# Kernel tuning notes

Hardware: AMD Instinct MI355X
Metric: run time of the kernel (lower is better)

Reference implementation:

```python
import jax, jax.numpy as jnp
import numpy as np


def _pairwise_sq_dists(x, y):
    # x: (B, N, 3), y: (B, M, 3) -> (B, N, M) squared L2 distances
    xx = jnp.sum(x * x, axis=2)                      # (B, N)
    yy = jnp.sum(y * y, axis=2)                      # (B, M)
    xy = jnp.einsum('bnd,bmd->bnm', x, y)            # (B, N, M)
    d = xx[:, :, None] + yy[:, None, :] - 2.0 * xy
    return jnp.maximum(d, 0.0)


def setup_inputs() -> dict:
    key = jax.random.key(0)
    k1, k2 = jax.random.split(key)
    B, N, M = 16, 4096, 4096
    pred = jax.random.normal(k1, (B, N, 3), dtype=jnp.float32)
    target = jax.random.normal(k2, (B, M, 3), dtype=jnp.float32)
    return {"pred": pred, "target": target}


def reference(pred, target):
    # ChamferLoss(use_l1=False, symmetry_weight=0.0), reduce='mean'
    d = _pairwise_sq_dists(pred, target)             # (B, N, M)
    min_p2t = jnp.min(d, axis=2)                     # (B, N)
    min_t2p = jnp.min(d, axis=1)                     # (B, M)
    per_sample = jnp.mean(min_p2t, axis=1) + jnp.mean(min_t2p, axis=1)  # (B,)
    return jnp.mean(per_sample)
```

## Files before the change

kernel.cpp:

```cpp
#include <hip/hip_runtime.h>
#include <math.h>

#define NPTS   4096
#define BATCH  16
#define BLK    512
#define CS     4
#define COLS_PER_BLK (NPTS / CS)
#define TPB    (COLS_PER_BLK / 32)
#define PANELS 16

typedef __attribute__((ext_vector_type(8)))  short bf16x8;
typedef __attribute__((ext_vector_type(16))) float f32x16;

static __device__ __forceinline__ unsigned short f2bf(float x) {
    unsigned u = __float_as_uint(x);
    unsigned r = 0x7FFFu + ((u >> 16) & 1u);
    return (unsigned short)((u + r) >> 16);
}
static __device__ __forceinline__ float bf2f(unsigned short h) {
    return __uint_as_float(((unsigned)h) << 16);
}
static __device__ __forceinline__ float min3f(float a, float b, float c) {
    return fminf(fminf(a, b), c);
}


__global__ __launch_bounds__(BLK) void chamfer_mfma(
    const float* __restrict__ pred, const float* __restrict__ target,
    unsigned* __restrict__ gcolmin, unsigned* __restrict__ growmin)
{
    __shared__ __align__(16) bf16x8 sB[TPB * 64];
    __shared__ unsigned colmin[COLS_PER_BLK];

    const int bx    = blockIdx.x;
    const int cs    = bx & (CS - 1);
    const int panel = bx >> 2;
    const int b     = blockIdx.y;
    const int t     = threadIdx.x;
    const int w     = t >> 6;
    const int l     = t & 63;
    const short one = (short)0x3F80;

    for (int i = t; i < COLS_PER_BLK; i += BLK) colmin[i] = 0x7F800000u;

    const int colbase = cs * COLS_PER_BLK;
    for (int e = t; e < TPB * 64; e += BLK) {
        const int el   = e & 63;
        const int tile = e >> 6;
        const int col  = colbase + tile * 32 + (el & 31);
        const float* tp = target + ((size_t)b * NPTS + col) * 3;
        float x = tp[0], y = tp[1], z = tp[2];
        unsigned short hx = f2bf(x), hy = f2bf(y), hz = f2bf(z);
        unsigned short lx = f2bf(x - bf2f(hx));
        unsigned short ly = f2bf(y - bf2f(hy));
        unsigned short lz = f2bf(z - bf2f(hz));
        float tt = fmaf(z, z, fmaf(y, y, x * x));
        unsigned short th = f2bf(tt);
        unsigned short tl = f2bf(tt - bf2f(th));
        bf16x8 v;
        if (el < 32)
            v = (bf16x8){(short)hx, (short)hy, (short)hz,
                         (short)hx, (short)hy, (short)hz,
                         (short)lx, (short)ly};
        else
            v = (bf16x8){(short)lz, one, one, (short)th, (short)tl, 0, 0, 0};
        sB[e] = v;
    }

    const int r   = l & 31;
    const int row = panel * 256 + w * 32 + r;
    const float* pp_ = pred + ((size_t)b * NPTS + row) * 3;
    float x = pp_[0], y = pp_[1], z = pp_[2];
    unsigned short hx = f2bf(x), hy = f2bf(y), hz = f2bf(z);
    unsigned short lx = f2bf(x - bf2f(hx));
    unsigned short ly = f2bf(y - bf2f(hy));
    unsigned short lz = f2bf(z - bf2f(hz));
    unsigned short n2hx = f2bf(-2.0f * bf2f(hx));
    unsigned short n2hy = f2bf(-2.0f * bf2f(hy));
    unsigned short n2hz = f2bf(-2.0f * bf2f(hz));
    unsigned short n2lx = f2bf(-2.0f * bf2f(lx));
    unsigned short n2ly = f2bf(-2.0f * bf2f(ly));
    unsigned short n2lz = f2bf(-2.0f * bf2f(lz));
    float pp = fmaf(z, z, fmaf(y, y, x * x));
    unsigned short pph = f2bf(pp);
    unsigned short ppl = f2bf(pp - bf2f(pph));
    bf16x8 afrag;
    if (l < 32)
        afrag = (bf16x8){(short)n2hx, (short)n2hy, (short)n2hz,
                         (short)n2lx, (short)n2ly, (short)n2lz,
                         (short)n2hx, (short)n2hy};
    else
        afrag = (bf16x8){(short)n2hz, (short)pph, (short)ppl, one, one, 0, 0, 0};

    __syncthreads();

    f32x16 rmin;
    #pragma unroll
    for (int i = 0; i < 16; ++i) rmin[i] = INFINITY;
    f32x16 zacc;
    #pragma unroll
    for (int i = 0; i < 16; ++i) zacc[i] = 0.0f;

    #pragma unroll 2
    for (int tile = 0; tile < TPB; ++tile) {
        bf16x8 bft = sB[tile * 64 + l];
        f32x16 acc = __builtin_amdgcn_mfma_f32_32x32x16_bf16(afrag, bft, zacc, 0, 0, 0);

        #pragma unroll
        for (int i = 0; i < 16; ++i) rmin[i] = fminf(rmin[i], acc[i]);

        float t0 = min3f(acc[0],  acc[1],  acc[2]);
        float t1 = min3f(acc[3],  acc[4],  acc[5]);
        float t2 = min3f(acc[6],  acc[7],  acc[8]);
        float t3 = min3f(acc[9],  acc[10], acc[11]);
        float t4 = min3f(acc[12], acc[13], acc[14]);
        float m  = fminf(min3f(t0, t1, t2), min3f(t3, t4, acc[15]));
        atomicMin(&colmin[tile * 32 + r], __float_as_uint(fmaxf(m, 0.0f)));
    }

    #pragma unroll
    for (int i = 0; i < 16; ++i) {
        float v = rmin[i];
        v = fminf(v, __shfl_xor(v, 1, 64));
        v = fminf(v, __shfl_xor(v, 2, 64));
        v = fminf(v, __shfl_xor(v, 4, 64));
        v = fminf(v, __shfl_xor(v, 8, 64));
        v = fminf(v, __shfl_xor(v, 16, 64));
        rmin[i] = v;
    }
    if ((l & 31) == 0) {
        const int h = l >> 5;
        unsigned* rb = growmin + (size_t)b * NPTS + panel * 256 + w * 32;
        #pragma unroll
        for (int i = 0; i < 16; ++i) {
            const int rloc = (i & 3) + 8 * (i >> 2) + 4 * h;
            atomicMin(&rb[rloc], __float_as_uint(fmaxf(rmin[i], 0.0f)));
        }
    }

    __syncthreads();
    unsigned* cb = gcolmin + (size_t)b * NPTS + colbase;
    for (int i = t; i < COLS_PER_BLK; i += BLK)
        atomicMin(&cb[i], colmin[i]);
}

__global__ __launch_bounds__(256) void chamfer_sum(
    const uint4* __restrict__ mins, float* __restrict__ out)
{
    __shared__ float wsum[4];
    const int gid = blockIdx.x * 256 + threadIdx.x;

    float s = 0.0f;
    for (int i = gid; i < (2 * BATCH * NPTS) / 4; i += 8192) {
        uint4 v = mins[i];
        s += __uint_as_float(v.x) + __uint_as_float(v.y)
           + __uint_as_float(v.z) + __uint_as_float(v.w);
    }

    #pragma unroll
    for (int off = 32; off > 0; off >>= 1)
        s += __shfl_down(s, off, 64);

    if ((threadIdx.x & 63) == 0) wsum[threadIdx.x >> 6] = s;
    __syncthreads();

    if (threadIdx.x == 0) {
        float acc = wsum[0] + wsum[1] + wsum[2] + wsum[3];
        atomicAdd(out, acc * (1.0f / ((float)BATCH * (float)NPTS)));
    }
}

extern "C" void kernel_launch(void* const* d_in, const int* in_sizes, int n_in,
                              void* d_out, int out_size, void* d_ws, size_t ws_size,
                              hipStream_t stream) {
    const float* pred   = (const float*)d_in[0];
    const float* target = (const float*)d_in[1];
    float* out = (float*)d_out;

    unsigned* gcolmin = (unsigned*)d_ws;
    unsigned* growmin = gcolmin + (size_t)BATCH * NPTS;

    hipMemsetAsync(d_ws, 0x7F, (size_t)2 * BATCH * NPTS * 4, stream);
    hipMemsetAsync(out, 0, sizeof(float), stream);

    chamfer_mfma<<<dim3(CS * PANELS, BATCH), BLK, 0, stream>>>(
        pred, target, gcolmin, growmin);
    chamfer_sum<<<dim3(32), 256, 0, stream>>>((const uint4*)d_ws, out);
}
```

Baseline: 82.71 us.

## Compute both Chamfer directions as row-min passes, drop atomics and memset

Instead of getting column minima through per-tile shared atomics, the kernel now adds a grid z dimension so each direction (pred→target and target→pred) runs as a pure row-min pass. Each wave holds two A fragments covering 64 rows, so every shared B tile load feeds two MFMAs. Per-column-split partial minima are written plainly, and the sum kernel folds the four splits, which removes the global atomicMin traffic and the workspace memset. The price is that the MFMA work doubles, since each pairwise distance is now computed once per direction.

```diff
diff --git a/kernel.cpp b/kernel.cpp
--- a/kernel.cpp
+++ b/kernel.cpp
@@ -7,7 +7,8 @@
 #define CS     4
 #define COLS_PER_BLK (NPTS / CS)
 #define TPB    (COLS_PER_BLK / 32)
-#define PANELS 16
+#define ROWS_PER_BLK 512
+#define PANELS (NPTS / ROWS_PER_BLK)
 
 typedef __attribute__((ext_vector_type(8)))  short bf16x8;
 typedef __attribute__((ext_vector_type(16))) float f32x16;
@@ -20,35 +21,57 @@
 static __device__ __forceinline__ float bf2f(unsigned short h) {
     return __uint_as_float(((unsigned)h) << 16);
 }
-static __device__ __forceinline__ float min3f(float a, float b, float c) {
-    return fminf(fminf(a, b), c);
+
+
+static __device__ __forceinline__ bf16x8 make_afrag(const float* mp, int l) {
+    const short one = (short)0x3F80;
+    float x = mp[0], y = mp[1], z = mp[2];
+    unsigned short hx = f2bf(x), hy = f2bf(y), hz = f2bf(z);
+    unsigned short lx = f2bf(x - bf2f(hx));
+    unsigned short ly = f2bf(y - bf2f(hy));
+    unsigned short lz = f2bf(z - bf2f(hz));
+    unsigned short n2hx = f2bf(-2.0f * bf2f(hx));
+    unsigned short n2hy = f2bf(-2.0f * bf2f(hy));
+    unsigned short n2hz = f2bf(-2.0f * bf2f(hz));
+    unsigned short n2lx = f2bf(-2.0f * bf2f(lx));
+    unsigned short n2ly = f2bf(-2.0f * bf2f(ly));
+    unsigned short n2lz = f2bf(-2.0f * bf2f(lz));
+    float pp = fmaf(z, z, fmaf(y, y, x * x));
+    unsigned short pph = f2bf(pp);
+    unsigned short ppl = f2bf(pp - bf2f(pph));
+    if (l < 32)
+        return (bf16x8){(short)n2hx, (short)n2hy, (short)n2hz,
+                        (short)n2lx, (short)n2ly, (short)n2lz,
+                        (short)n2hx, (short)n2hy};
+    else
+        return (bf16x8){(short)n2hz, (short)pph, (short)ppl, one, one, 0, 0, 0};
 }
-
 
 __global__ __launch_bounds__(BLK) void chamfer_mfma(
     const float* __restrict__ pred, const float* __restrict__ target,
-    unsigned* __restrict__ gcolmin, unsigned* __restrict__ growmin)
+    float* __restrict__ partial)
 {
     __shared__ __align__(16) bf16x8 sB[TPB * 64];
-    __shared__ unsigned colmin[COLS_PER_BLK];
 
     const int bx    = blockIdx.x;
     const int cs    = bx & (CS - 1);
     const int panel = bx >> 2;
     const int b     = blockIdx.y;
+    const int dir   = blockIdx.z;
     const int t     = threadIdx.x;
     const int w     = t >> 6;
     const int l     = t & 63;
     const short one = (short)0x3F80;
 
-    for (int i = t; i < COLS_PER_BLK; i += BLK) colmin[i] = 0x7F800000u;
+    const float* mine  = dir ? target : pred;
+    const float* other = dir ? pred : target;
 
     const int colbase = cs * COLS_PER_BLK;
     for (int e = t; e < TPB * 64; e += BLK) {
         const int el   = e & 63;
         const int tile = e >> 6;
         const int col  = colbase + tile * 32 + (el & 31);
-        const float* tp = target + ((size_t)b * NPTS + col) * 3;
+        const float* tp = other + ((size_t)b * NPTS + col) * 3;
         float x = tp[0], y = tp[1], z = tp[2];
         unsigned short hx = f2bf(x), hy = f2bf(y), hz = f2bf(z);
         unsigned short lx = f2bf(x - bf2f(hx));
@@ -67,94 +90,72 @@
         sB[e] = v;
     }
 
-    const int r   = l & 31;
-    const int row = panel * 256 + w * 32 + r;
-    const float* pp_ = pred + ((size_t)b * NPTS + row) * 3;
-    float x = pp_[0], y = pp_[1], z = pp_[2];
-    unsigned short hx = f2bf(x), hy = f2bf(y), hz = f2bf(z);
-    unsigned short lx = f2bf(x - bf2f(hx));
-    unsigned short ly = f2bf(y - bf2f(hy));
-    unsigned short lz = f2bf(z - bf2f(hz));
-    unsigned short n2hx = f2bf(-2.0f * bf2f(hx));
-    unsigned short n2hy = f2bf(-2.0f * bf2f(hy));
-    unsigned short n2hz = f2bf(-2.0f * bf2f(hz));
-    unsigned short n2lx = f2bf(-2.0f * bf2f(lx));
-    unsigned short n2ly = f2bf(-2.0f * bf2f(ly));
-    unsigned short n2lz = f2bf(-2.0f * bf2f(lz));
-    float pp = fmaf(z, z, fmaf(y, y, x * x));
-    unsigned short pph = f2bf(pp);
-    unsigned short ppl = f2bf(pp - bf2f(pph));
-    bf16x8 afrag;
-    if (l < 32)
-        afrag = (bf16x8){(short)n2hx, (short)n2hy, (short)n2hz,
-                         (short)n2lx, (short)n2ly, (short)n2lz,
-                         (short)n2hx, (short)n2hy};
-    else
-        afrag = (bf16x8){(short)n2hz, (short)pph, (short)ppl, one, one, 0, 0, 0};
+    const int rowbase = panel * ROWS_PER_BLK + w * 64;
+    const size_t mb = (size_t)b * NPTS;
+    bf16x8 af[2];
+    #pragma unroll
+    for (int j = 0; j < 2; ++j)
+        af[j] = make_afrag(mine + (mb + rowbase + j * 32 + (l & 31)) * 3, l);
 
     __syncthreads();
 
-    f32x16 rmin;
+    f32x16 rm[2];
     #pragma unroll
-    for (int i = 0; i < 16; ++i) rmin[i] = INFINITY;
+    for (int j = 0; j < 2; ++j)
+        #pragma unroll
+        for (int i = 0; i < 16; ++i) rm[j][i] = INFINITY;
+
     f32x16 zacc;
     #pragma unroll
     for (int i = 0; i < 16; ++i) zacc[i] = 0.0f;
 
-    #pragma unroll 2
     for (int tile = 0; tile < TPB; ++tile) {
         bf16x8 bft = sB[tile * 64 + l];
-        f32x16 acc = __builtin_amdgcn_mfma_f32_32x32x16_bf16(afrag, bft, zacc, 0, 0, 0);
-
+        f32x16 a0 = __builtin_amdgcn_mfma_f32_32x32x16_bf16(af[0], bft, zacc, 0, 0, 0);
+        f32x16 a1 = __builtin_amdgcn_mfma_f32_32x32x16_bf16(af[1], bft, zacc, 0, 0, 0);
         #pragma unroll
-        for (int i = 0; i < 16; ++i) rmin[i] = fminf(rmin[i], acc[i]);
-
-        float t0 = min3f(acc[0],  acc[1],  acc[2]);
-        float t1 = min3f(acc[3],  acc[4],  acc[5]);
-        float t2 = min3f(acc[6],  acc[7],  acc[8]);
-        float t3 = min3f(acc[9],  acc[10], acc[11]);
-        float t4 = min3f(acc[12], acc[13], acc[14]);
-        float m  = fminf(min3f(t0, t1, t2), min3f(t3, t4, acc[15]));
-        atomicMin(&colmin[tile * 32 + r], __float_as_uint(fmaxf(m, 0.0f)));
+        for (int i = 0; i < 16; ++i) rm[0][i] = fminf(rm[0][i], a0[i]);
+        #pragma unroll
+        for (int i = 0; i < 16; ++i) rm[1][i] = fminf(rm[1][i], a1[i]);
     }
 
+    const int h = l >> 5;
+    float* pb = partial + (((size_t)dir * BATCH + b) * CS + cs) * NPTS;
     #pragma unroll
-    for (int i = 0; i < 16; ++i) {
-        float v = rmin[i];
-        v = fminf(v, __shfl_xor(v, 1, 64));
-        v = fminf(v, __shfl_xor(v, 2, 64));
-        v = fminf(v, __shfl_xor(v, 4, 64));
-        v = fminf(v, __shfl_xor(v, 8, 64));
-        v = fminf(v, __shfl_xor(v, 16, 64));
-        rmin[i] = v;
-    }
-    if ((l & 31) == 0) {
-        const int h = l >> 5;
-        unsigned* rb = growmin + (size_t)b * NPTS + panel * 256 + w * 32;
+    for (int j = 0; j < 2; ++j) {
         #pragma unroll
         for (int i = 0; i < 16; ++i) {
-            const int rloc = (i & 3) + 8 * (i >> 2) + 4 * h;
-            atomicMin(&rb[rloc], __float_as_uint(fmaxf(rmin[i], 0.0f)));
+            float v = rm[j][i];
+            v = fminf(v, __shfl_xor(v, 1, 64));
+            v = fminf(v, __shfl_xor(v, 2, 64));
+            v = fminf(v, __shfl_xor(v, 4, 64));
+            v = fminf(v, __shfl_xor(v, 8, 64));
+            v = fminf(v, __shfl_xor(v, 16, 64));
+            rm[j][i] = v;
+        }
+        if ((l & 31) == 0) {
+            #pragma unroll
+            for (int i = 0; i < 16; ++i) {
+                const int row = rowbase + j * 32 + (i & 3) + 8 * (i >> 2) + 4 * h;
+                pb[row] = rm[j][i];
+            }
         }
     }
-
-    __syncthreads();
-    unsigned* cb = gcolmin + (size_t)b * NPTS + colbase;
-    for (int i = t; i < COLS_PER_BLK; i += BLK)
-        atomicMin(&cb[i], colmin[i]);
 }
 
 __global__ __launch_bounds__(256) void chamfer_sum(
-    const uint4* __restrict__ mins, float* __restrict__ out)
+    const float* __restrict__ partial, float* __restrict__ out)
 {
     __shared__ float wsum[4];
     const int gid = blockIdx.x * 256 + threadIdx.x;
 
     float s = 0.0f;
-    for (int i = gid; i < (2 * BATCH * NPTS) / 4; i += 8192) {
-        uint4 v = mins[i];
-        s += __uint_as_float(v.x) + __uint_as_float(v.y)
-           + __uint_as_float(v.z) + __uint_as_float(v.w);
+    for (int i = gid; i < 2 * BATCH * NPTS; i += 8192) {
+        const int db  = i >> 12;
+        const int row = i & (NPTS - 1);
+        const float* p = partial + (size_t)db * CS * NPTS + row;
+        float v = fminf(fminf(p[0], p[NPTS]), fminf(p[2 * NPTS], p[3 * NPTS]));
+        s += fmaxf(v, 0.0f);
     }
 
     #pragma unroll
@@ -176,14 +177,11 @@
     const float* pred   = (const float*)d_in[0];
     const float* target = (const float*)d_in[1];
     float* out = (float*)d_out;
+    float* partial = (float*)d_ws;
 
-    unsigned* gcolmin = (unsigned*)d_ws;
-    unsigned* growmin = gcolmin + (size_t)BATCH * NPTS;
-
-    hipMemsetAsync(d_ws, 0x7F, (size_t)2 * BATCH * NPTS * 4, stream);
     hipMemsetAsync(out, 0, sizeof(float), stream);
 
-    chamfer_mfma<<<dim3(CS * PANELS, BATCH), BLK, 0, stream>>>(
-        pred, target, gcolmin, growmin);
-    chamfer_sum<<<dim3(32), 256, 0, stream>>>((const uint4*)d_ws, out);
+    chamfer_mfma<<<dim3(CS * PANELS, BATCH, 2), BLK, 0, stream>>>(
+        pred, target, partial);
+    chamfer_sum<<<dim3(32), 256, 0, stream>>>(partial, out);
 }
```

New measurement: 92.17 us. 1.11x slower.
